# Optimization experiments

Measured on AMD Instinct MI355X. Metric: run time of the kernel, lower is better.

Reference implementation:

```python
import jax, jax.numpy as jnp
from jax import lax
import numpy as np

B, V = 2, 6
C_IN, HF, WF = 64, 32, 56
ND = 32
BEV_C, BEV_H, BEV_W = 128, 128, 128
D_MIN, D_MAX, EXT = 1.0, 50.0, 20.0
BN_S = 1.0 / np.sqrt(1.0 + 1e-5)  # BatchNorm at init (running mean=0, var=1): x / sqrt(1+eps)

def _conv(x, w, b, pad):
    y = lax.conv_general_dilated(x, w, (1, 1), [(pad, pad), (pad, pad)],
                                 dimension_numbers=('NCHW', 'OIHW', 'NCHW'))
    return y + b[None, :, None, None]

def _gelu(x):
    return jax.nn.gelu(x, approximate=False)  # torch nn.GELU default = exact erf

def setup_inputs() -> dict:
    key = jax.random.key(0)
    ks = jax.random.split(key, 8)
    feat_maps = jax.random.normal(ks[0], (B, V, C_IN, HF, WF), jnp.float32)
    # pinhole intrinsics at feature-map scale
    f = 30.0
    K1 = np.array([[f, 0.0, WF / 2.0], [0.0, f, HF / 2.0], [0.0, 0.0, 1.0]], np.float32)
    K = jnp.broadcast_to(jnp.asarray(K1), (B, V, 3, 3))
    # cam->ego extrinsics: cam optical frame (x right, y down, z fwd) -> ego, yaw per camera
    R0 = np.array([[0., 0., 1.], [-1., 0., 0.], [0., -1., 0.]], np.float32)
    Ts = np.zeros((B, V, 4, 4), np.float32)
    for v in range(V):
        yaw = 2.0 * np.pi * v / V
        Rz = np.array([[np.cos(yaw), -np.sin(yaw), 0.], [np.sin(yaw), np.cos(yaw), 0.], [0., 0., 1.]], np.float32)
        Ts[:, v, :3, :3] = Rz @ R0
        Ts[:, v, :3, 3] = np.array([0.0, 0.0, 1.5], np.float32)
        Ts[:, v, 3, 3] = 1.0
    T = jnp.asarray(Ts)
    trust = jax.random.uniform(ks[1], (B, V), jnp.float32)
    depths = jnp.linspace(D_MIN, D_MAX, ND).astype(jnp.float32)
    s = 0.05
    dh_w1 = jax.random.normal(ks[2], (C_IN, C_IN, 3, 3), jnp.float32) * s
    dh_b1 = jnp.zeros((C_IN,), jnp.float32)
    dh_w2 = jax.random.normal(ks[3], (ND, C_IN, 1, 1), jnp.float32) * s
    dh_b2 = jnp.zeros((ND,), jnp.float32)
    fp_w = jax.random.normal(ks[4], (BEV_C, C_IN, 1, 1), jnp.float32) * s
    fp_b = jnp.zeros((BEV_C,), jnp.float32)
    br_w1 = jax.random.normal(ks[5], (BEV_C, BEV_C, 3, 3), jnp.float32) * s
    br_b1 = jnp.zeros((BEV_C,), jnp.float32)
    br_w2 = jax.random.normal(ks[6], (BEV_C, BEV_C, 3, 3), jnp.float32) * s
    br_b2 = jnp.zeros((BEV_C,), jnp.float32)
    return dict(feat_maps=feat_maps, K=K, T=T, trust=trust, depths=depths,
                dh_w1=dh_w1, dh_b1=dh_b1, dh_w2=dh_w2, dh_b2=dh_b2,
                fp_w=fp_w, fp_b=fp_b, br_w1=br_w1, br_b1=br_b1, br_w2=br_w2, br_b2=br_b2)

def reference(feat_maps, K, T, trust, depths, dh_w1, dh_b1, dh_w2, dh_b2, fp_w, fp_b, br_w1, br_b1, br_w2, br_b2):
    Bq, Vq, C, Hf, Wf = feat_maps.shape
    fm = feat_maps.reshape(Bq * Vq, C, Hf, Wf)
    # depth head -> per-pixel categorical over depth bins
    h = _gelu(_conv(fm, dh_w1, dh_b1, 1) * BN_S)
    depth_probs = jax.nn.softmax(_conv(h, dh_w2, dh_b2, 0), axis=1)   # (BV, ND, Hf, Wf)
    fp = _gelu(_conv(fm, fp_w, fp_b, 0) * BN_S)                       # (BV, Cb, Hf, Wf)
    feat_vox = fp[:, :, None] * depth_probs[:, None]                  # (BV, Cb, ND, Hf, Wf)
    Cb = fp.shape[1]
    Dn = depths.shape[0]
    Np = Hf * Wf * Dn
    # torch order: permute(0,2,3,1) -> (Cb, Hf, Wf, ND) flattened as (h, w, d)
    fv = feat_vox.transpose(0, 1, 3, 4, 2).reshape(Bq, Vq, Cb, Np)
    # frustum points in camera frame, same (pixel, depth) ordering
    yy, xx = jnp.meshgrid(jnp.arange(Hf, dtype=jnp.float32), jnp.arange(Wf, dtype=jnp.float32), indexing='ij')
    pix = jnp.stack([xx.ravel(), yy.ravel(), jnp.ones(Hf * Wf, jnp.float32)], axis=0)  # (3, P)
    Kinv = jnp.linalg.inv(K)                                          # (B,V,3,3)
    rays = jnp.einsum('bvij,jp->bvip', Kinv, pix)                     # (B,V,3,P)
    pts = rays[..., None] * depths                                    # (B,V,3,P,D)
    R = T[..., :3, :3]
    t = T[..., :3, 3]
    pts_ego = jnp.einsum('bvij,bvjpd->bvipd', R, pts) + t[..., None, None]
    x_e = pts_ego[:, :, 0].reshape(Bq, Vq, Np)
    y_e = pts_ego[:, :, 1].reshape(Bq, Vq, Np)
    col = ((x_e + EXT) / (2.0 * EXT) * (BEV_W - 1)).astype(jnp.int32)  # trunc-toward-zero == torch .long()
    row = ((y_e + EXT) / (2.0 * EXT) * (BEV_H - 1)).astype(jnp.int32)
    valid = (col >= 0) & (col < BEV_W) & (row >= 0) & (row < BEV_H)
    idx = jnp.where(valid, row * BEV_W + col, 0)                      # (B,V,Np)
    tw = lax.stop_gradient(trust)                                     # torch uses trust[b,v].item()
    contrib = fv * (tw[:, :, None, None] * valid[:, :, None, :].astype(fv.dtype))
    HWb = BEV_H * BEV_W
    idx_all = (idx + jnp.arange(Bq)[:, None, None] * HWb).reshape(-1)
    contrib_flat = contrib.transpose(2, 0, 1, 3).reshape(Cb, -1)      # (Cb, B*V*Np)
    bev_flat = jnp.zeros((Cb, Bq * HWb), fv.dtype).at[:, idx_all].add(contrib_flat)
    bev = bev_flat.reshape(Cb, Bq, BEV_H, BEV_W).transpose(1, 0, 2, 3)  # (B, Cb, H, W)
    h2 = _gelu(_conv(bev, br_w1, br_b1, 1) * BN_S)
    out = _gelu(_conv(h2, br_w2, br_b2, 1) * BN_S)
    return out
```

## Files before the change

### kernel.cpp

```cpp
#include <hip/hip_runtime.h>
#include <hip/hip_bf16.h>
#include <math.h>

#define BQ 2
#define NV 6
#define CIN 64
#define HF 32
#define WF 56
#define ND 32
#define BEVC 128
#define BEVH 128
#define BEVW 128
#define NPIX (HF*WF)
#define BV (BQ*NV)
#define NCOL (BV*WF)
#define NITEM (NCOL*ND)
#define NCELL (BQ*BEVH*BEVW)
#define BCAP 16
#define EXT 20.0f
#define BN_S 0.99999500003749937f

typedef short bf16x8 __attribute__((ext_vector_type(8)));
typedef float f32x4 __attribute__((ext_vector_type(4)));

__device__ __forceinline__ float gelu(float x) {
    return 0.5f * x * (1.0f + erff(x * 0.70710678118654752f));
}

__device__ __forceinline__ unsigned short f2bf(float x) {
    union { float f; unsigned u; } v; v.f = x;
    unsigned r = v.u + 0x7FFFu + ((v.u >> 16) & 1u);
    return (unsigned short)(r >> 16);
}

__device__ void atomicAddBf16(unsigned short* addr, float val) {
    unsigned* base = (unsigned*)((size_t)addr & ~(size_t)3);
    bool hi = ((size_t)addr & 2) != 0;
    unsigned old = *base, assumed;
    do {
        assumed = old;
        unsigned short cur = hi ? (unsigned short)(assumed >> 16)
                                : (unsigned short)(assumed & 0xFFFF);
        union { unsigned u; float f; } vv; vv.u = ((unsigned)cur) << 16;
        unsigned short nb = f2bf(vv.f + val);
        unsigned newv = hi ? ((assumed & 0x0000FFFFu) | ((unsigned)nb << 16))
                           : ((assumed & 0xFFFF0000u) | (unsigned)nb);
        old = atomicCAS(base, assumed, newv);
    } while (old != assumed);
}

#define WF1_N (9*4*8*64*8)
#define WFP_N (2*8*64*8)
#define WFC1_N (9*2*4*64*8)
__global__ void k_wprep_all(const float* __restrict__ br_w1, const float* __restrict__ br_w2,
                            const float* __restrict__ fp_w, const float* __restrict__ dh_w1,
                            unsigned short* __restrict__ wf1, unsigned short* __restrict__ wf2,
                            unsigned short* __restrict__ wfp, unsigned short* __restrict__ wfc1,
                            int* __restrict__ count, int* __restrict__ ovf_n) {
    int gi = blockIdx.x * 256 + threadIdx.x;
    if (gi < NCELL) count[gi] = 0;
    if (gi == 0) *ovf_n = 0;

    int i = gi;
    if (i < 2 * WF1_N) {
        const float* w = (i < WF1_N) ? br_w1 : br_w2;
        unsigned short* wf = (i < WF1_N) ? wf1 : wf2;
        int j = (i < WF1_N) ? i : i - WF1_N;
        int e     = j & 7;
        int lane  = (j >> 3) & 63;
        int ntile = (j >> 9) & 7;
        int kstep = (j >> 12) & 3;
        int kpos  = j >> 14;
        int co = ntile * 16 + (lane & 15);
        int ci = kstep * 32 + ((lane >> 4) << 3) + e;
        wf[j] = f2bf(w[((size_t)co * BEVC + ci) * 9 + kpos]);
        return;
    }
    i -= 2 * WF1_N;
    if (i < WFP_N) {
        int e     = i & 7;
        int lane  = (i >> 3) & 63;
        int ntile = (i >> 9) & 7;
        int kstep = (i >> 12) & 1;
        int co = ntile * 16 + (lane & 15);
        int ci = kstep * 32 + ((lane >> 4) << 3) + e;
        wfp[i] = f2bf(fp_w[(size_t)co * CIN + ci]);
        return;
    }
    i -= WFP_N;
    if (i < WFC1_N) {
        int e     = i & 7;
        int lane  = (i >> 3) & 63;
        int ntile = (i >> 9) & 3;
        int kstep = (i >> 11) & 1;
        int kpos  = i >> 12;
        int co = ntile * 16 + (lane & 15);
        int ci = kstep * 32 + ((lane >> 4) << 3) + e;
        wfc1[i] = f2bf(dh_w1[((size_t)co * CIN + ci) * 9 + kpos]);
    }
}

#define C1_HW 18
#define C1_HP (C1_HW*6)
__global__ void k_conv1dfp(const float* __restrict__ fm, const unsigned short* __restrict__ wfrag,
                           const float* __restrict__ bias, const float* __restrict__ w2,
                           const float* __restrict__ b2, const unsigned short* __restrict__ wfp,
                           const float* __restrict__ fp_b,
                           float* __restrict__ dp, float* __restrict__ fpb) {
    __shared__ float hbuf[64 * 65];
    __shared__ float wl2[ND * 65];
    __shared__ float bl2[ND];
    char* als = (char*)hbuf;

    int x0 = blockIdx.x * 16;
    int y0 = blockIdx.y * 4;
    int bv = blockIdx.z;
    const float* fmb = fm + (size_t)bv * CIN * NPIX;

    for (int i = threadIdx.x; i < ND * CIN; i += 256) {
        int d = i >> 6, ci = i & 63;
        wl2[d * 65 + ci] = w2[i];
    }
    if (threadIdx.x < ND) bl2[threadIdx.x] = b2[threadIdx.x];

    for (int i = threadIdx.x; i < C1_HP * 8; i += 256) {
        int pix = i >> 3, oct = i & 7;
        int r = pix / C1_HW, c = pix % C1_HW;
        int gy = y0 + r - 1, gx = x0 + c - 1;
        int4 w4 = {0, 0, 0, 0};
        if ((unsigned)gy < (unsigned)HF && (unsigned)gx < (unsigned)WF) {
            const float* p = fmb + (size_t)(oct * 8) * NPIX + gy * WF + gx;
            unsigned short b8[8];
            #pragma unroll
            for (int j = 0; j < 8; j++) b8[j] = f2bf(p[(size_t)j * NPIX]);
            w4.x = b8[0] | ((int)b8[1] << 16);
            w4.y = b8[2] | ((int)b8[3] << 16);
            w4.z = b8[4] | ((int)b8[5] << 16);
            w4.w = b8[6] | ((int)b8[7] << 16);
        }
        *(int4*)(als + pix * 128 + ((oct * 16) ^ ((pix & 7) << 4))) = w4;
    }
    __syncthreads();

    int wave = threadIdx.x >> 6;
    int lane = threadIdx.x & 63;
    int xx   = lane & 15;
    int kgrp = lane >> 4;

    const bf16x8* wv = (const bf16x8*)wfrag;
    float bi = bias[wave * 16 + xx];
    f32x4 acc[4];
    #pragma unroll
    for (int m = 0; m < 4; m++) acc[m] = (f32x4){bi, bi, bi, bi};

    for (int kpos = 0; kpos < 9; kpos++) {
        int dy = kpos / 3, dx = kpos % 3;
        #pragma unroll
        for (int kstep = 0; kstep < 2; kstep++) {
            bf16x8 b = wv[((kpos * 2 + kstep) * 4 + wave) * 64 + lane];
            #pragma unroll
            for (int m = 0; m < 4; m++) {
                int pix = (m + dy) * C1_HW + xx + dx;
                bf16x8 a = *(const bf16x8*)(als + pix * 128 +
                                            ((kstep * 64 + kgrp * 16) ^ ((pix & 7) << 4)));
                acc[m] = __builtin_amdgcn_mfma_f32_16x16x32_bf16(a, b, acc[m], 0, 0, 0);
            }
        }
    }

    {
        const bf16x8* wvp = (const bf16x8*)wfp;
        int hpix = (wave + 1) * C1_HW + xx + 1;
        bf16x8 fa0 = *(const bf16x8*)(als + hpix * 128 +
                                      ((       kgrp * 16) ^ ((hpix & 7) << 4)));
        bf16x8 fa1 = *(const bf16x8*)(als + hpix * 128 +
                                      ((64 +   kgrp * 16) ^ ((hpix & 7) << 4)));
        #pragma unroll
        for (int n = 0; n < 8; n++) {
            float fb = fp_b[n * 16 + xx];
            f32x4 facc = (f32x4){fb, fb, fb, fb};
            facc = __builtin_amdgcn_mfma_f32_16x16x32_bf16(fa0, wvp[(0 * 8 + n) * 64 + lane], facc, 0, 0, 0);
            facc = __builtin_amdgcn_mfma_f32_16x16x32_bf16(fa1, wvp[(1 * 8 + n) * 64 + lane], facc, 0, 0, 0);
            #pragma unroll
            for (int r = 0; r < 4; r++) {
                int gx = x0 + kgrp * 4 + r;
                if (gx < WF)
                    fpb[((size_t)bv * NPIX + (y0 + wave) * WF + gx) * BEVC + n * 16 + xx] =
                        gelu(facc[r] * BN_S);
            }
        }
    }
    __syncthreads();

    #pragma unroll
    for (int m = 0; m < 4; m++) {
        #pragma unroll
        for (int r = 0; r < 4; r++) {
            int pixel = m * 16 + kgrp * 4 + r;
            hbuf[pixel * 65 + wave * 16 + xx] = gelu(acc[m][r] * BN_S);
        }
    }
    __syncthreads();

    {
        int pixel = threadIdx.x >> 2;
        int part  = threadIdx.x & 3;
        int m = pixel >> 4, xcol = pixel & 15;
        int gy = y0 + m, gx = x0 + xcol;

        float hv[CIN];
        #pragma unroll
        for (int c4 = 0; c4 < CIN / 4; c4++) {
            float4 v = *(const float4*)&hbuf[pixel * 65 + c4 * 4];
            hv[c4 * 4 + 0] = v.x; hv[c4 * 4 + 1] = v.y;
            hv[c4 * 4 + 2] = v.z; hv[c4 * 4 + 3] = v.w;
        }
        float o[8];
        float mx = -1e30f;
        #pragma unroll
        for (int dd = 0; dd < 8; dd++) {
            int d = part * 8 + dd;
            float a = bl2[d];
            #pragma unroll
            for (int ci = 0; ci < CIN; ci++) a += wl2[d * 65 + ci] * hv[ci];
            o[dd] = a;
            mx = fmaxf(mx, a);
        }
        mx = fmaxf(mx, __shfl_xor(mx, 1));
        mx = fmaxf(mx, __shfl_xor(mx, 2));
        float s = 0.f;
        #pragma unroll
        for (int dd = 0; dd < 8; dd++) { o[dd] = expf(o[dd] - mx); s += o[dd]; }
        s += __shfl_xor(s, 1);
        s += __shfl_xor(s, 2);
        float inv = 1.0f / s;
        if (gx < WF) {
            float* op = dp + ((size_t)bv * NPIX + gy * WF + gx) * ND + part * 8;
            float4 v0 = {o[0] * inv, o[1] * inv, o[2] * inv, o[3] * inv};
            float4 v1 = {o[4] * inv, o[5] * inv, o[6] * inv, o[7] * inv};
            ((float4*)op)[0] = v0;
            ((float4*)op)[1] = v1;
        }
    }
}

struct Geo {
    float i00,i01,i02,i10,i11,i12,i20,i21,i22;
    float R00,R01,R02,t0,R10,R11,R12,t1;
};
__device__ __forceinline__ Geo load_geo(const float* Km, const float* Tm, int bv) {
    Geo G;
    const float* Kp = Km + bv * 9;
    float a = Kp[0], bb = Kp[1], cc = Kp[2];
    float d = Kp[3], e  = Kp[4], f  = Kp[5];
    float g = Kp[6], hh = Kp[7], ii = Kp[8];
    float A  = e * ii - f * hh;
    float Bm = -(d * ii - f * g);
    float Cm = d * hh - e * g;
    float det = a * A + bb * Bm + cc * Cm;
    float invd = 1.0f / det;
    G.i00 = A * invd;  G.i01 = -(bb * ii - cc * hh) * invd; G.i02 = (bb * f - cc * e) * invd;
    G.i10 = Bm * invd; G.i11 = (a * ii - cc * g) * invd;    G.i12 = -(a * f - cc * d) * invd;
    G.i20 = Cm * invd; G.i21 = -(a * hh - bb * g) * invd;   G.i22 = (a * e - bb * d) * invd;
    const float* Tp = Tm + bv * 16;
    G.R00 = Tp[0]; G.R01 = Tp[1]; G.R02 = Tp[2]; G.t0 = Tp[3];
    G.R10 = Tp[4]; G.R11 = Tp[5]; G.R12 = Tp[6]; G.t1 = Tp[7];
    return G;
}
__device__ __forceinline__ int geo_cell(const Geo& G, int px, int py, float dep) {
    float fx = (float)px, fy = (float)py;
    float r0 = G.i00 * fx + G.i01 * fy + G.i02;
    float r1 = G.i10 * fx + G.i11 * fy + G.i12;
    float r2 = G.i20 * fx + G.i21 * fy + G.i22;
    float xe = G.R00 * (r0 * dep) + G.R01 * (r1 * dep) + G.R02 * (r2 * dep) + G.t0;
    float ye = G.R10 * (r0 * dep) + G.R11 * (r1 * dep) + G.R12 * (r2 * dep) + G.t1;
    int col = (int)((xe + EXT) / (2.0f * EXT) * (float)(BEVW - 1));
    int row = (int)((ye + EXT) / (2.0f * EXT) * (float)(BEVH - 1));
    return (col >= 0 && col < BEVW && row >= 0 && row < BEVH) ? row * BEVW + col : -1;
}

__global__ void k_prered(const float* __restrict__ fp, const float* __restrict__ dp,
                         const float* __restrict__ Km, const float* __restrict__ Tm,
                         const float* __restrict__ trust, const float* __restrict__ depths,
                         float* __restrict__ M, int* __restrict__ cellidx,
                         int* __restrict__ count, int* __restrict__ bucket,
                         int* __restrict__ ovf, int* __restrict__ ovf_n) {
    __shared__ float fpl[HF * BEVC];
    __shared__ float dpl[HF * ND];
    __shared__ int   celll[ND * HF];
    __shared__ int   uni[ND];

    int col = blockIdx.x;
    int bv = col / WF, px = col % WF;
    int b  = bv / NV;
    float tw = trust[bv];

    for (int i = threadIdx.x; i < HF * (BEVC / 4); i += 256) {
        int py = i >> 5, c4 = i & 31;
        float4 v = ((const float4*)(fp + ((size_t)bv * NPIX + py * WF + px) * BEVC))[c4];
        v.x *= tw; v.y *= tw; v.z *= tw; v.w *= tw;
        ((float4*)fpl)[py * 32 + c4] = v;
    }
    for (int i = threadIdx.x; i < HF * (ND / 4); i += 256) {
        int py = i >> 3, d4 = i & 7;
        ((float4*)dpl)[py * 8 + d4] =
            ((const float4*)(dp + ((size_t)bv * NPIX + py * WF + px) * ND))[d4];
    }

    Geo G = load_geo(Km, Tm, bv);
    for (int q = threadIdx.x; q < ND * HF; q += 256) {
        int di = q >> 5, py = q & 31;
        celll[q] = geo_cell(G, px, py, depths[di]);
    }
    __syncthreads();

    if (threadIdx.x < ND) {
        int di = threadIdx.x;
        int c0 = celll[di * HF];
        bool u = true;
        for (int py = 1; py < HF; py++) u &= (celll[di * HF + py] == c0);
        uni[di] = u ? c0 : -2;
    }
    __syncthreads();

    int c = threadIdx.x & 127, dg = threadIdx.x >> 7;
    float acc[16];
    #pragma unroll
    for (int k = 0; k < 16; k++) acc[k] = 0.f;
    for (int py = 0; py < HF; py++) {
        float fv = fpl[py * BEVC + c];
        #pragma unroll
        for (int k = 0; k < 16; k++)
            acc[k] += fv * dpl[py * ND + dg * 16 + k];
    }
    #pragma unroll
    for (int k = 0; k < 16; k++)
        M[((size_t)col * ND + dg * 16 + k) * BEVC + c] = acc[k];

    if (threadIdx.x < ND) {
        int u = uni[threadIdx.x];
        int id = (u >= 0) ? (b * (BEVH * BEVW) + u) : u;
        int item = col * ND + threadIdx.x;
        cellidx[item] = id;
        if (id >= 0) {
            int slot = atomicAdd(&count[id], 1);
            if (slot < BCAP) bucket[id * BCAP + slot] = item;
            else             ovf[atomicAdd(ovf_n, 1)] = item;
        }
    }
}

__global__ void k_gather(const float* __restrict__ M, const int* __restrict__ count,
                         const int* __restrict__ bucket, unsigned short* __restrict__ bev) {
    int cell = blockIdx.x;
    int n = count[cell];
    if (n > BCAP) n = BCAP;
    int c = threadIdx.x;
    float acc = 0.f;
    for (int j = 0; j < n; j++) {
        int it = bucket[cell * BCAP + j];
        acc += M[(size_t)it * BEVC + c];
    }
    bev[(size_t)cell * BEVC + c] = f2bf(acc);
}

__global__ void k_ovf(const float* __restrict__ M, const int* __restrict__ cellidx,
                      const int* __restrict__ ovf, const int* __restrict__ ovf_n,
                      unsigned short* __restrict__ bev) {
    int no = *ovf_n;
    int c = threadIdx.x;
    for (int i = blockIdx.x; i < no; i += gridDim.x) {
        int it = ovf[i];
        int cell = cellidx[it];
        atomicAddBf16(&bev[(size_t)cell * BEVC + c], M[(size_t)it * BEVC + c]);
    }
}

__global__ void k_fallback(const float* __restrict__ fp, const float* __restrict__ dp,
                           const float* __restrict__ Km, const float* __restrict__ Tm,
                           const float* __restrict__ trust, const float* __restrict__ depths,
                           const int* __restrict__ cellidx, unsigned short* __restrict__ bev) {
    int col = blockIdx.x;
    bool any = false;
    for (int di = 0; di < ND; di++) any |= (cellidx[col * ND + di] == -2);
    if (!any) return;

    int bv = col / WF, px = col % WF;
    int b  = bv / NV;
    float tw = trust[bv];
    Geo G = load_geo(Km, Tm, bv);
    int c = threadIdx.x;
    unsigned short* bevb = bev + (size_t)b * BEVH * BEVW * BEVC;
    for (int di = 0; di < ND; di++) {
        if (cellidx[col * ND + di] != -2) continue;
        float dep = depths[di];
        for (int py = 0; py < HF; py++) {
            int cell = geo_cell(G, px, py, dep);
            if (cell >= 0) {
                float v = fp[((size_t)bv * NPIX + py * WF + px) * BEVC + c] * tw *
                          dp[((size_t)bv * NPIX + py * WF + px) * ND + di];
                atomicAddBf16(&bevb[(size_t)cell * BEVC + c], v);
            }
        }
    }
}

#define TX2 16
#define TY2 4
#define HALO_W 18
#define HP (HALO_W*6)

__device__ __forceinline__ int swz(int pix, int off) {
    return pix * 256 + (off ^ ((pix & 7) << 4));
}

template<int TO_MODE>
__global__ __launch_bounds__(256, 2)
void k_bevconv(const unsigned short* __restrict__ in_,
               const unsigned short* __restrict__ wfrag,
               const float* __restrict__ bias, void* __restrict__ out_) {
    __shared__ char ldsb[HP * 256];
    int bid = blockIdx.x;
    int id = (bid & 7) * 64 + (bid >> 3);
    int x0 = (id & 7) * TX2;
    int y0 = ((id >> 3) & 31) * TY2;
    int b  = id >> 8;

    for (int t = threadIdx.x; t < HP * 16; t += 256) {
        int pix = t >> 4, oct = t & 15;
        int r = pix / HALO_W, c = pix % HALO_W;
        int gy = y0 + r - 1, gx = x0 + c - 1;
        int4 w4 = {0, 0, 0, 0};
        if ((unsigned)gy < (unsigned)BEVH && (unsigned)gx < (unsigned)BEVW)
            w4 = *(const int4*)(in_ + ((size_t)(b * BEVH + gy) * BEVW + gx) * BEVC + oct * 8);
        *(int4*)(ldsb + swz(pix, oct * 16)) = w4;
    }

    int wave = threadIdx.x >> 6;
    int lane = threadIdx.x & 63;
    int xx   = lane & 15;
    int kgrp = lane >> 4;

    const bf16x8* wv = (const bf16x8*)wfrag;
    int wbase = wave * 2;

    bf16x8 wq[4][2];
    #pragma unroll
    for (int p = 0; p < 4; p++) {
        wq[p][0] = wv[(p * 8 + wbase + 0) * 64 + lane];
        wq[p][1] = wv[(p * 8 + wbase + 1) * 64 + lane];
    }

    f32x4 acc[TY2][2];
    {
        float b0 = bias[wave * 32 + xx];
        float b1 = bias[wave * 32 + 16 + xx];
        #pragma unroll
        for (int m = 0; m < TY2; m++) {
            acc[m][0] = (f32x4){b0, b0, b0, b0};
            acc[m][1] = (f32x4){b1, b1, b1, b1};
        }
    }
    __syncthreads();

    #pragma unroll
    for (int i = 0; i < 36; i++) {
        const int kpos = i >> 2, kstep = i & 3;
        const int dy = kpos / 3, dx = kpos % 3;
        bf16x8 b0 = wq[i & 3][0];
        bf16x8 b1 = wq[i & 3][1];
        if (i + 4 < 36) {
            wq[i & 3][0] = wv[((i + 4) * 8 + wbase + 0) * 64 + lane];
            wq[i & 3][1] = wv[((i + 4) * 8 + wbase + 1) * 64 + lane];
        }
        #pragma unroll
        for (int m = 0; m < TY2; m++) {
            bf16x8 a = *(const bf16x8*)(ldsb + swz((m + dy) * HALO_W + xx + dx,
                                                   kstep * 64 + kgrp * 16));
            acc[m][0] = __builtin_amdgcn_mfma_f32_16x16x32_bf16(a, b0, acc[m][0], 0, 0, 0);
            acc[m][1] = __builtin_amdgcn_mfma_f32_16x16x32_bf16(a, b1, acc[m][1], 0, 0, 0);
        }
    }
    __syncthreads();

    if (TO_MODE == 1) {
        unsigned short* hl = (unsigned short*)ldsb;
        #pragma unroll
        for (int m = 0; m < TY2; m++)
            #pragma unroll
            for (int n = 0; n < 2; n++)
                #pragma unroll
                for (int r = 0; r < 4; r++) {
                    int pid = m * 16 + kgrp * 4 + r;
                    hl[pid * 136 + wave * 32 + n * 16 + xx] = f2bf(gelu(acc[m][n][r] * BN_S));
                }
        __syncthreads();
        for (int t = threadIdx.x; t < 1024; t += 256) {
            int pid = t >> 4, oct = t & 15;
            int gy = y0 + (pid >> 4), gx = x0 + (pid & 15);
            *(int4*)((unsigned short*)out_ + ((size_t)(b * BEVH + gy) * BEVW + gx) * BEVC + oct * 8) =
                *(int4*)(hl + pid * 136 + oct * 8);
        }
    } else {
        float* fl = (float*)ldsb;
        #pragma unroll
        for (int half = 0; half < 2; half++) {
            if (half == 1) __syncthreads();
            if ((wave >> 1) == half) {
                #pragma unroll
                for (int m = 0; m < TY2; m++)
                    #pragma unroll
                    for (int n = 0; n < 2; n++)
                        #pragma unroll
                        for (int r = 0; r < 4; r++) {
                            int pid = m * 16 + kgrp * 4 + r;
                            fl[pid * 66 + (wave & 1) * 32 + n * 16 + xx] =
                                gelu(acc[m][n][r] * BN_S);
                        }
            }
            __syncthreads();
            for (int t = threadIdx.x; t < 1024; t += 256) {
                int l4 = t & 3, gyl = (t >> 2) & 3, col = t >> 4;
                int co = half * 64 + col;
                int gy = y0 + gyl;
                float4 v;
                v.x = fl[(gyl * 16 + l4 * 4 + 0) * 66 + col];
                v.y = fl[(gyl * 16 + l4 * 4 + 1) * 66 + col];
                v.z = fl[(gyl * 16 + l4 * 4 + 2) * 66 + col];
                v.w = fl[(gyl * 16 + l4 * 4 + 3) * 66 + col];
                *(float4*)((float*)out_ + (((size_t)b * BEVC + co) * BEVH + gy) * BEVW +
                           x0 + l4 * 4) = v;
            }
        }
    }
}

extern "C" void kernel_launch(void* const* d_in, const int* in_sizes, int n_in,
                              void* d_out, int out_size, void* d_ws, size_t ws_size,
                              hipStream_t stream) {
    const float* feat_maps = (const float*)d_in[0];
    const float* Km        = (const float*)d_in[1];
    const float* Tm        = (const float*)d_in[2];
    const float* trust     = (const float*)d_in[3];
    const float* depths    = (const float*)d_in[4];
    const float* dh_w1     = (const float*)d_in[5];
    const float* dh_b1     = (const float*)d_in[6];
    const float* dh_w2     = (const float*)d_in[7];
    const float* dh_b2     = (const float*)d_in[8];
    const float* fp_w      = (const float*)d_in[9];
    const float* fp_b      = (const float*)d_in[10];
    const float* br_w1     = (const float*)d_in[11];
    const float* br_b1     = (const float*)d_in[12];
    const float* br_w2     = (const float*)d_in[13];
    const float* br_b2     = (const float*)d_in[14];
    float* out = (float*)d_out;

    float* ws  = (float*)d_ws;
    float* dpb = ws;
    float* fpb = dpb + (size_t)BV * NPIX * ND;
    float* Mb  = fpb + (size_t)BV * NPIX * BEVC;
    unsigned short* bevb = (unsigned short*)(Mb + (size_t)NITEM * BEVC);
    unsigned short* h2b  = bevb + (size_t)NCELL * BEVC;
    unsigned short* wf1  = h2b + (size_t)NCELL * BEVC;
    unsigned short* wf2  = wf1 + (size_t)WF1_N;
    unsigned short* wfp  = wf2 + (size_t)WF1_N;
    unsigned short* wfc1 = wfp + WFP_N;
    int* cellidx  = (int*)(wfc1 + WFC1_N);
    int* count    = cellidx + NITEM;
    int* bucket   = count + NCELL;
    int* ovf      = bucket + NCELL * BCAP;
    int* ovf_n    = ovf + NITEM;

    {
        int total = 2 * WF1_N + WFP_N + WFC1_N;
        k_wprep_all<<<dim3((total + 255) / 256), dim3(256), 0, stream>>>(
            br_w1, br_w2, fp_w, dh_w1, wf1, wf2, wfp, wfc1, count, ovf_n);
    }

    k_conv1dfp<<<dim3(4, HF / 4, BV), dim3(256), 0, stream>>>(
        feat_maps, wfc1, dh_b1, dh_w2, dh_b2, wfp, fp_b, dpb, fpb);

    k_prered<<<dim3(NCOL), dim3(256), 0, stream>>>(fpb, dpb, Km, Tm, trust, depths,
                                                   Mb, cellidx, count, bucket, ovf, ovf_n);
    k_gather<<<dim3(NCELL), dim3(BEVC), 0, stream>>>(Mb, count, bucket, bevb);
    k_ovf<<<dim3(64), dim3(BEVC), 0, stream>>>(Mb, cellidx, ovf, ovf_n, bevb);
    k_fallback<<<dim3(NCOL), dim3(BEVC), 0, stream>>>(fpb, dpb, Km, Tm, trust, depths,
                                                      cellidx, bevb);

    k_bevconv<1><<<dim3(512), dim3(256), 0, stream>>>(bevb, wf1, br_b1, h2b);
    k_bevconv<2><<<dim3(512), dim3(256), 0, stream>>>(h2b, wf2, br_b2, out);
}
```

Before: 111.1 us.

## Fuse the two BEV 3x3 convolutions into one kernel with halo recompute

The two back-to-back 3x3 BEV convolutions now run in a single kernel. Each block loads a 20x8 input halo, computes the first conv on an 18x6 intermediate tile (including a 1-pixel halo, recomputed redundantly by neighbours), stores it as bf16 in LDS, then runs the second conv from LDS. This removes the h2 global round-trip and one launch. In exchange it spends extra MFMA work on the intermediate halo (7 vs 4 m-tiles in conv1), holds more accumulator registers, and needs larger LDS, which may reduce occupancy.

```diff
diff --git a/kernel.cpp b/kernel.cpp
--- a/kernel.cpp
+++ b/kernel.cpp
@@ -405,61 +405,67 @@
     }
 }
 
-#define TX2 16
-#define TY2 4
-#define HALO_W 18
-#define HP (HALO_W*6)
-
-__device__ __forceinline__ int swz(int pix, int off) {
-    return pix * 256 + (off ^ ((pix & 7) << 4));
-}
-
-template<int TO_MODE>
+#define H2W 20
+#define H2P (H2W*8)
+#define IW 18
+#define IP (IW*6)
+
 __global__ __launch_bounds__(256, 2)
-void k_bevconv(const unsigned short* __restrict__ in_,
-               const unsigned short* __restrict__ wfrag,
-               const float* __restrict__ bias, void* __restrict__ out_) {
-    __shared__ char ldsb[HP * 256];
+void k_bevconv2x(const unsigned short* __restrict__ in_,
+                 const unsigned short* __restrict__ wf1, const float* __restrict__ b1,
+                 const unsigned short* __restrict__ wf2, const float* __restrict__ b2,
+                 float* __restrict__ out_) {
+    __shared__ char lds[H2P * 256 + IP * 256];
+    char* rA = lds;
+    char* rB = lds + H2P * 256;
+
     int bid = blockIdx.x;
     int id = (bid & 7) * 64 + (bid >> 3);
-    int x0 = (id & 7) * TX2;
-    int y0 = ((id >> 3) & 31) * TY2;
+    int x0 = (id & 7) * 16;
+    int y0 = ((id >> 3) & 31) * 4;
     int b  = id >> 8;
 
-    for (int t = threadIdx.x; t < HP * 16; t += 256) {
+    for (int t = threadIdx.x; t < H2P * 16; t += 256) {
         int pix = t >> 4, oct = t & 15;
-        int r = pix / HALO_W, c = pix % HALO_W;
-        int gy = y0 + r - 1, gx = x0 + c - 1;
+        int r = pix / H2W, c = pix % H2W;
+        int gy = y0 + r - 2, gx = x0 + c - 2;
         int4 w4 = {0, 0, 0, 0};
         if ((unsigned)gy < (unsigned)BEVH && (unsigned)gx < (unsigned)BEVW)
             w4 = *(const int4*)(in_ + ((size_t)(b * BEVH + gy) * BEVW + gx) * BEVC + oct * 8);
-        *(int4*)(ldsb + swz(pix, oct * 16)) = w4;
+        *(int4*)(rA + pix * 256 + ((oct * 16) ^ ((pix & 7) << 4))) = w4;
     }
 
     int wave = threadIdx.x >> 6;
     int lane = threadIdx.x & 63;
     int xx   = lane & 15;
     int kgrp = lane >> 4;
-
-    const bf16x8* wv = (const bf16x8*)wfrag;
     int wbase = wave * 2;
 
+    const bf16x8* wv1 = (const bf16x8*)wf1;
+    const bf16x8* wv2 = (const bf16x8*)wf2;
+
+    int pbase[7];
+    #pragma unroll
+    for (int mt = 0; mt < 7; mt++) {
+        int p = mt * 16 + xx;
+        int pr = p / IW, pc = p % IW;
+        pbase[mt] = pr * H2W + pc;
+    }
+
     bf16x8 wq[4][2];
     #pragma unroll
     for (int p = 0; p < 4; p++) {
-        wq[p][0] = wv[(p * 8 + wbase + 0) * 64 + lane];
-        wq[p][1] = wv[(p * 8 + wbase + 1) * 64 + lane];
-    }
-
-    f32x4 acc[TY2][2];
-    {
-        float b0 = bias[wave * 32 + xx];
-        float b1 = bias[wave * 32 + 16 + xx];
-        #pragma unroll
-        for (int m = 0; m < TY2; m++) {
-            acc[m][0] = (f32x4){b0, b0, b0, b0};
-            acc[m][1] = (f32x4){b1, b1, b1, b1};
-        }
+        wq[p][0] = wv1[(p * 8 + wbase + 0) * 64 + lane];
+        wq[p][1] = wv1[(p * 8 + wbase + 1) * 64 + lane];
+    }
+
+    float c1b0 = b1[wave * 32 + xx];
+    float c1b1 = b1[wave * 32 + 16 + xx];
+    f32x4 acc1[7][2];
+    #pragma unroll
+    for (int mt = 0; mt < 7; mt++) {
+        acc1[mt][0] = (f32x4){c1b0, c1b0, c1b0, c1b0};
+        acc1[mt][1] = (f32x4){c1b1, c1b1, c1b1, c1b1};
     }
     __syncthreads();
 
@@ -468,47 +474,88 @@
         const int kpos = i >> 2, kstep = i & 3;
         const int dy = kpos / 3, dx = kpos % 3;
         bf16x8 b0 = wq[i & 3][0];
-        bf16x8 b1 = wq[i & 3][1];
+        bf16x8 b1v = wq[i & 3][1];
         if (i + 4 < 36) {
-            wq[i & 3][0] = wv[((i + 4) * 8 + wbase + 0) * 64 + lane];
-            wq[i & 3][1] = wv[((i + 4) * 8 + wbase + 1) * 64 + lane];
-        }
-        #pragma unroll
-        for (int m = 0; m < TY2; m++) {
-            bf16x8 a = *(const bf16x8*)(ldsb + swz((m + dy) * HALO_W + xx + dx,
-                                                   kstep * 64 + kgrp * 16));
+            wq[i & 3][0] = wv1[((i + 4) * 8 + wbase + 0) * 64 + lane];
+            wq[i & 3][1] = wv1[((i + 4) * 8 + wbase + 1) * 64 + lane];
+        }
+        #pragma unroll
+        for (int mt = 0; mt < 7; mt++) {
+            int inpix = pbase[mt] + dy * H2W + dx;
+            bf16x8 a = *(const bf16x8*)(rA + inpix * 256 +
+                                        ((kstep * 64 + kgrp * 16) ^ ((inpix & 7) << 4)));
+            acc1[mt][0] = __builtin_amdgcn_mfma_f32_16x16x32_bf16(a, b0, acc1[mt][0], 0, 0, 0);
+            acc1[mt][1] = __builtin_amdgcn_mfma_f32_16x16x32_bf16(a, b1v, acc1[mt][1], 0, 0, 0);
+        }
+    }
+
+    #pragma unroll
+    for (int mt = 0; mt < 7; mt++) {
+        #pragma unroll
+        for (int n = 0; n < 2; n++) {
+            int co = wave * 32 + n * 16 + xx;
+            #pragma unroll
+            for (int rr = 0; rr < 4; rr++) {
+                int pp = mt * 16 + kgrp * 4 + rr;
+                if (pp < IP) {
+                    int pr = pp / IW, pc = pp % IW;
+                    int gy = y0 + pr - 1, gx = x0 + pc - 1;
+                    unsigned short v = 0;
+                    if ((unsigned)gy < (unsigned)BEVH && (unsigned)gx < (unsigned)BEVW)
+                        v = f2bf(gelu(acc1[mt][n][rr] * BN_S));
+                    *(unsigned short*)(rB + pp * 256 + ((co * 2) ^ ((pp & 7) << 4))) = v;
+                }
+            }
+        }
+    }
+
+    #pragma unroll
+    for (int p = 0; p < 4; p++) {
+        wq[p][0] = wv2[(p * 8 + wbase + 0) * 64 + lane];
+        wq[p][1] = wv2[(p * 8 + wbase + 1) * 64 + lane];
+    }
+
+    f32x4 acc[4][2];
+    {
+        float bb0 = b2[wave * 32 + xx];
+        float bb1 = b2[wave * 32 + 16 + xx];
+        #pragma unroll
+        for (int m = 0; m < 4; m++) {
+            acc[m][0] = (f32x4){bb0, bb0, bb0, bb0};
+            acc[m][1] = (f32x4){bb1, bb1, bb1, bb1};
+        }
+    }
+    __syncthreads();
+
+    #pragma unroll
+    for (int i = 0; i < 36; i++) {
+        const int kpos = i >> 2, kstep = i & 3;
+        const int dy = kpos / 3, dx = kpos % 3;
+        bf16x8 b0 = wq[i & 3][0];
+        bf16x8 b1v = wq[i & 3][1];
+        if (i + 4 < 36) {
+            wq[i & 3][0] = wv2[((i + 4) * 8 + wbase + 0) * 64 + lane];
+            wq[i & 3][1] = wv2[((i + 4) * 8 + wbase + 1) * 64 + lane];
+        }
+        #pragma unroll
+        for (int m = 0; m < 4; m++) {
+            int inpix = (m + dy) * IW + xx + dx;
+            bf16x8 a = *(const bf16x8*)(rB + inpix * 256 +
+                                        ((kstep * 64 + kgrp * 16) ^ ((inpix & 7) << 4)));
             acc[m][0] = __builtin_amdgcn_mfma_f32_16x16x32_bf16(a, b0, acc[m][0], 0, 0, 0);
-            acc[m][1] = __builtin_amdgcn_mfma_f32_16x16x32_bf16(a, b1, acc[m][1], 0, 0, 0);
-        }
-    }
-    __syncthreads();
-
-    if (TO_MODE == 1) {
-        unsigned short* hl = (unsigned short*)ldsb;
-        #pragma unroll
-        for (int m = 0; m < TY2; m++)
-            #pragma unroll
-            for (int n = 0; n < 2; n++)
-                #pragma unroll
-                for (int r = 0; r < 4; r++) {
-                    int pid = m * 16 + kgrp * 4 + r;
-                    hl[pid * 136 + wave * 32 + n * 16 + xx] = f2bf(gelu(acc[m][n][r] * BN_S));
-                }
-        __syncthreads();
-        for (int t = threadIdx.x; t < 1024; t += 256) {
-            int pid = t >> 4, oct = t & 15;
-            int gy = y0 + (pid >> 4), gx = x0 + (pid & 15);
-            *(int4*)((unsigned short*)out_ + ((size_t)(b * BEVH + gy) * BEVW + gx) * BEVC + oct * 8) =
-                *(int4*)(hl + pid * 136 + oct * 8);
-        }
-    } else {
-        float* fl = (float*)ldsb;
+            acc[m][1] = __builtin_amdgcn_mfma_f32_16x16x32_bf16(a, b1v, acc[m][1], 0, 0, 0);
+        }
+    }
+    __syncthreads();
+
+    {
+        float* fl = (float*)rA;
         #pragma unroll
         for (int half = 0; half < 2; half++) {
             if (half == 1) __syncthreads();
             if ((wave >> 1) == half) {
                 #pragma unroll
-                for (int m = 0; m < TY2; m++)
+                for (int m = 0; m < 4; m++)
                     #pragma unroll
                     for (int n = 0; n < 2; n++)
                         #pragma unroll
@@ -528,8 +575,7 @@
                 v.y = fl[(gyl * 16 + l4 * 4 + 1) * 66 + col];
                 v.z = fl[(gyl * 16 + l4 * 4 + 2) * 66 + col];
                 v.w = fl[(gyl * 16 + l4 * 4 + 3) * 66 + col];
-                *(float4*)((float*)out_ + (((size_t)b * BEVC + co) * BEVH + gy) * BEVW +
-                           x0 + l4 * 4) = v;
+                *(float4*)(out_ + (((size_t)b * BEVC + co) * BEVH + gy) * BEVW + x0 + l4 * 4) = v;
             }
         }
     }
@@ -560,8 +606,7 @@
     float* fpb = dpb + (size_t)BV * NPIX * ND;
     float* Mb  = fpb + (size_t)BV * NPIX * BEVC;
     unsigned short* bevb = (unsigned short*)(Mb + (size_t)NITEM * BEVC);
-    unsigned short* h2b  = bevb + (size_t)NCELL * BEVC;
-    unsigned short* wf1  = h2b + (size_t)NCELL * BEVC;
+    unsigned short* wf1  = bevb + (size_t)NCELL * BEVC;
     unsigned short* wf2  = wf1 + (size_t)WF1_N;
     unsigned short* wfp  = wf2 + (size_t)WF1_N;
     unsigned short* wfc1 = wfp + WFP_N;
@@ -587,6 +632,5 @@
     k_fallback<<<dim3(NCOL), dim3(BEVC), 0, stream>>>(fpb, dpb, Km, Tm, trust, depths,
                                                       cellidx, bevb);
 
-    k_bevconv<1><<<dim3(512), dim3(256), 0, stream>>>(bevb, wf1, br_b1, h2b);
-    k_bevconv<2><<<dim3(512), dim3(256), 0, stream>>>(h2b, wf2, br_b2, out);
-}
+    k_bevconv2x<<<dim3(512), dim3(256), 0, stream>>>(bevb, wf1, br_b1, wf2, br_b2, out);
+}
```

Result: no change. 113.2 us (+1.9%).
